# Optimization experiments

Hardware: AMD Instinct MI355X
Metric: run time of the kernel (lower is better)

The kernel has to match this reference:

```python
import jax, jax.numpy as jnp
import numpy as np
from jax import lax

NB_DIGITS = 2
BASE = 10
NUMS = BASE ** NB_DIGITS            # 100 possible values per number
SUMS = 2 * (NUMS - 1) + 1           # 199 possible sums (circuit roots)
B = 4096                            # logical batch size
N_IMAGES = B * 2 * NB_DIGITS        # 16384 digit images


def setup_inputs() -> dict:
    key = jax.random.key(0)
    ks = jax.random.split(key, 11)
    s = 0.1
    return {
        "images": jax.random.normal(ks[0], (N_IMAGES, 1, 28, 28), jnp.float32),
        "conv1_w": jax.random.normal(ks[1], (6, 1, 5, 5), jnp.float32) * s,
        "conv1_b": jax.random.normal(ks[2], (6,), jnp.float32) * s,
        "conv2_w": jax.random.normal(ks[3], (16, 6, 5, 5), jnp.float32) * s,
        "conv2_b": jax.random.normal(ks[4], (16,), jnp.float32) * s,
        "fc1_w": jax.random.normal(ks[5], (120, 256), jnp.float32) * s,
        "fc1_b": jax.random.normal(ks[6], (120,), jnp.float32) * s,
        "fc2_w": jax.random.normal(ks[7], (84, 120), jnp.float32) * s,
        "fc2_b": jax.random.normal(ks[8], (84,), jnp.float32) * s,
        "fc3_w": jax.random.normal(ks[9], (10, 84), jnp.float32) * s,
        "fc3_b": jax.random.normal(ks[10], (10,), jnp.float32) * s,
    }


def _conv(x, w, b):
    y = lax.conv_general_dilated(x, w, (1, 1), 'VALID',
                                 dimension_numbers=('NCHW', 'OIHW', 'NCHW'))
    return y + b[None, :, None, None]


def _maxpool2(x):
    return lax.reduce_window(x, -jnp.inf, lax.max, (1, 1, 2, 2), (1, 1, 2, 2), 'VALID')


def _lenet(x, c1w, c1b, c2w, c2b, f1w, f1b, f2w, f2b, f3w, f3b):
    x = jax.nn.relu(_maxpool2(_conv(x, c1w, c1b)))   # [N,6,12,12]
    x = jax.nn.relu(_maxpool2(_conv(x, c2w, c2b)))   # [N,16,4,4]
    x = x.reshape(-1, 16 * 4 * 4)
    x = jax.nn.relu(x @ f1w.T + f1b)
    x = jax.nn.relu(x @ f2w.T + f2b)
    x = x @ f3w.T + f3b
    return jax.nn.log_softmax(x, axis=-1)            # [N,10]


def _circuit(lp):
    # lp: [B, 2*NB_DIGITS, 10] per-digit log-probs.
    # Vars layout from get_circuit: positions 0..NB_DIGITS-1 = n1 digits (MSB first),
    # positions NB_DIGITS..2*NB_DIGITS-1 = n2 digits. Neg-literal weights are 0 in
    # log space (the `zeros` arg), so each model's weight = sum of digit log-probs;
    # OR over models = logsumexp grouped by n1+n2.
    d = jnp.arange(NUMS)
    hi, lo = d // BASE, d % BASE
    lp1 = lp[:, 0, hi] + lp[:, 1, lo]                # [B, NUMS] log P(n1=k)
    lp2 = lp[:, 2, hi] + lp[:, 3, lo]                # [B, NUMS] log P(n2=k)
    M = (lp1[:, :, None] + lp2[:, None, :]).reshape(lp.shape[0], -1)  # [B, NUMS^2]
    seg = (jnp.arange(NUMS)[:, None] + jnp.arange(NUMS)[None, :]).reshape(-1)
    Mf = M.T                                          # [NUMS^2, B]
    m = jax.ops.segment_max(Mf, seg, num_segments=SUMS)              # [SUMS, B]
    ssum = jax.ops.segment_sum(jnp.exp(Mf - m[seg]), seg, num_segments=SUMS)
    return (jnp.log(ssum) + m).T                      # [B, SUMS] log P(sum=s)


def reference(images, conv1_w, conv1_b, conv2_w, conv2_b,
              fc1_w, fc1_b, fc2_w, fc2_b, fc3_w, fc3_b):
    logp = _lenet(images, conv1_w, conv1_b, conv2_w, conv2_b,
                  fc1_w, fc1_b, fc2_w, fc2_b, fc3_w, fc3_b)   # [N_IMAGES,10]
    lp = logp.reshape(B, 2 * NB_DIGITS, BASE)
    return _circuit(lp)
```

## Files before the change

### kernel.cpp

```cpp
#include <hip/hip_runtime.h>
#include <hip/hip_bf16.h>
#include <math.h>

#define SUMS 199
#define NBLK 1024

typedef __attribute__((ext_vector_type(8))) short short8;
typedef __attribute__((ext_vector_type(4))) float float4v;

union Frag8 { short8 v; unsigned u[4]; uint4 q; };

static __device__ inline unsigned pk_bf16(float a, float b) {
    __hip_bfloat162 h = __float22bfloat162_rn(make_float2(a, b));
    union { __hip_bfloat162 h; unsigned u; } c; c.h = h; return c.u;
}

__global__ __launch_bounds__(256) void convert_weights(
    const float* __restrict__ f1w, const float* __restrict__ f2w,
    const float* __restrict__ f3w, const float* __restrict__ c1w,
    const float* __restrict__ c2w, uint4* __restrict__ ws)
{
    const int g = blockIdx.x * 256 + threadIdx.x;
    if (g >= 6400) return;
    float v[8];
    if (g < 5824) {
        const float* W; int O, K, ld, nt, s, l;
        if (g < 4096)      { W = f1w; O = 120; K = 256; ld = 256; nt = g >> 9; s = (g >> 6) & 7; l = g & 63; }
        else if (g < 5632) { const int f = g - 4096; W = f2w; O = 84; K = 120; ld = 120; nt = f >> 8; s = (f >> 6) & 3; l = f & 63; }
        else               { const int f = g - 5632; W = f3w; O = 10; K = 84;  ld = 84;  nt = 0; s = f >> 6; l = f & 63; }
        const int o = nt * 16 + (l & 15);
        #pragma unroll
        for (int j = 0; j < 8; ++j) {
            const int k = 32 * s + 8 * (l >> 4) + j;
            v[j] = (o < O && k < K) ? W[o * ld + k] : 0.f;
        }
    } else if (g < 6336) {
        const int f = g - 5824, s = f >> 6, l = f & 63;
        const int c = l & 15, h = l >> 4;
        #pragma unroll
        for (int jp = 0; jp < 4; ++jp) {
            const int D = 16 * s + 4 * h + jp;
            const int ky = D / 24, rem = D % 24, kx = rem >> 2, icp = rem & 3;
            const bool ok = (ky < 5 && kx < 5);
            v[2 * jp]     = (ok && 2 * icp < 6)     ? c2w[c * 150 + (2 * icp) * 25 + ky * 5 + kx]     : 0.f;
            v[2 * jp + 1] = (ok && 2 * icp + 1 < 6) ? c2w[c * 150 + (2 * icp + 1) * 25 + ky * 5 + kx] : 0.f;
        }
    } else {
        const int l = (g - 6336) & 63;
        const int c = l & 15, h = l >> 4;
        const int oc = c >> 1, xs = c & 1;
        #pragma unroll
        for (int j = 0; j < 8; ++j) {
            const int p = h * 4 + (j >> 1);
            float w = 0.f;
            if (p < 15 && c < 12) {
                const int ky = p / 3, kx = 2 * (p % 3) + (j & 1) - xs;
                if (kx >= 0 && kx < 5) w = c1w[oc * 25 + ky * 5 + kx];
            }
            v[j] = w;
        }
    }
    uint4 r;
    r.x = pk_bf16(v[0], v[1]); r.y = pk_bf16(v[2], v[3]);
    r.z = pk_bf16(v[4], v[5]); r.w = pk_bf16(v[6], v[7]);
    ws[g] = r;
}

__global__ __launch_bounds__(256) void lenet_circuit_kernel(
    const float* __restrict__ images,
    const float* __restrict__ c1b, const float* __restrict__ c2b,
    const float* __restrict__ f1b, const float* __restrict__ f2b,
    const float* __restrict__ f3b, const uint4* __restrict__ wsb,
    float* __restrict__ out)
{
    __shared__ __align__(16) unsigned char s_mem[39712];
    unsigned*       imgu = (unsigned*)s_mem;
    unsigned short* p1s  = (unsigned short*)(s_mem + 12576);
    const uint4*    p1u4 = (const uint4*)(s_mem + 12576);
    unsigned*       A1d  = (unsigned*)(s_mem + 31264);
    const uint4*    A1q  = (const uint4*)(s_mem + 31264);
    float*          pgf  = (float*)(s_mem + 7680);
    float*          Hf   = (float*)(s_mem + 8448);
    float*          Lf   = (float*)(s_mem + 8768);

    const int t = threadIdx.x, bid = blockIdx.x;
    const int lane = t & 63, wav = t >> 6;
    const int c = lane & 15, h = lane >> 4;
    const uint4 z4 = {0u, 0u, 0u, 0u};

    {
        uint4* pz = (uint4*)(s_mem + 12576);
        for (int i = t; i < 1168; i += 256) pz[i] = z4;
    }
    Frag8 a1; a1.q = wsb[6336 + lane];
    Frag8 w2[8];
    #pragma unroll
    for (int s = 0; s < 8; ++s) w2[s].q = wsb[5824 + s * 64 + lane];
    int koff[8];
    #pragma unroll
    for (int s = 0; s < 8; ++s) {
        const int D0 = 16 * s + 4 * h;
        koff[s] = (D0 / 24) * 12 + ((D0 % 24) >> 2);
    }
    int pd[4];
    #pragma unroll
    for (int q = 0; q < 4; ++q) {
        const int p = 4 * h + q;
        pd[q] = (p < 15) ? (p / 3) * 14 + (p % 3) : 0;
    }
    float bias0 = 0.f, bias1 = 0.f;
    if (h < 3) { bias0 = c1b[2 * h]; bias1 = c1b[2 * h + 1]; }
    const float b2v = c2b[c];

    for (int pass = 0; pass < 2; ++pass) {
        {
            const float4* g = (const float4*)(images + (size_t)bid * 12544 + pass * 6272);
            for (int i = t; i < 1568; i += 256) {
                const float4 v = g[i];
                const int im = i / 196, j = i % 196;
                imgu[im * 393 + 2 * j]     = pk_bf16(v.x, v.y);
                imgu[im * 393 + 2 * j + 1] = pk_bf16(v.z, v.w);
            }
        }
        __syncthreads();

        {
            const int n = c, img = n >> 1;
            const int imb = img * 393 + (n & 1) * 14;
            for (int qy = wav * 3; qy < wav * 3 + 3; ++qy) {
                #pragma unroll
                for (int qx = 0; qx < 12; ++qx) {
                    const int base = imb + qy * 28 + qx;
                    Frag8 bf;
                    #pragma unroll
                    for (int q = 0; q < 4; ++q) bf.u[q] = imgu[base + pd[q]];
                    float4v acc = {0.f, 0.f, 0.f, 0.f};
                    acc = __builtin_amdgcn_mfma_f32_16x16x32_bf16(a1.v, bf.v, acc, 0, 0, 0);
                    float v0 = fmaxf(acc[0], acc[1]);
                    float v1 = fmaxf(acc[2], acc[3]);
                    v0 = fmaxf(v0, __shfl_xor(v0, 1));
                    v1 = fmaxf(v1, __shfl_xor(v1, 1));
                    if ((n & 1) == 0 && h < 3) {
                        const unsigned pkv = pk_bf16(fmaxf(v0 + bias0, 0.f),
                                                     fmaxf(v1 + bias1, 0.f));
                        *(unsigned*)&p1s[img * 1152 + qy * 96 + qx * 8 + 2 * h] = pkv;
                    }
                }
            }
        }
        __syncthreads();

        {
            const int pxl = (c & 1) + 2 * ((c >> 2) & 1);
            const int pyl = ((c >> 1) & 1) + 2 * ((c >> 3) & 1);
            #pragma unroll
            for (int ii = 0; ii < 2; ++ii) {
                const int i0 = 2 * wav + ii;
                #pragma unroll
                for (int mt = 0; mt < 4; ++mt) {
                    const int px = pxl + 4 * (mt & 1), py = pyl + 4 * (mt >> 1);
                    const int base = i0 * 144 + py * 12 + px;
                    float4v acc = {0.f, 0.f, 0.f, 0.f};
                    #pragma unroll
                    for (int s = 0; s < 8; ++s) {
                        Frag8 af; af.q = p1u4[base + koff[s]];
                        acc = __builtin_amdgcn_mfma_f32_16x16x32_bf16(af.v, w2[s].v, acc, 0, 0, 0);
                    }
                    const float p = fmaxf(fmaxf(acc[0], acc[1]), fmaxf(acc[2], acc[3]));
                    float v = fmaxf(p + b2v, 0.f);
                    const float vp = __shfl_xor(v, 16);
                    if ((h & 1) == 0) {
                        const int qy = (h >> 1) + 2 * (mt >> 1);
                        A1d[(pass * 8 + i0) * 132 + c * 8 + qy * 2 + (mt & 1)] = pk_bf16(v, vp);
                    }
                }
            }
        }
    }
    __syncthreads();

    {
        unsigned* A2d = (unsigned*)s_mem;
        if (t < 64) A2d[(t >> 2) * 68 + 60 + (t & 3)] = 0u;
        float4v acc0 = {0.f, 0.f, 0.f, 0.f}, acc1 = acc0;
        const int nt0 = 2 * wav;
        #pragma unroll
        for (int s = 0; s < 8; ++s) {
            Frag8 af; af.q = A1q[c * 33 + 4 * s + h];
            Frag8 b0; b0.q = wsb[(nt0 * 8 + s) * 64 + lane];
            Frag8 b1; b1.q = wsb[((nt0 + 1) * 8 + s) * 64 + lane];
            acc0 = __builtin_amdgcn_mfma_f32_16x16x32_bf16(af.v, b0.v, acc0, 0, 0, 0);
            acc1 = __builtin_amdgcn_mfma_f32_16x16x32_bf16(af.v, b1.v, acc1, 0, 0, 0);
        }
        #pragma unroll
        for (int ntl = 0; ntl < 2; ++ntl) {
            const int o = 32 * wav + 16 * ntl + c;
            const float bias = (o < 120) ? f1b[o] : 0.f;
            #pragma unroll
            for (int r = 0; r < 4; ++r) {
                float v = fmaxf((ntl ? acc1[r] : acc0[r]) + bias, 0.f);
                const float vp = __shfl_xor(v, 1);
                if ((c & 1) == 0 && o < 120)
                    A2d[(4 * h + r) * 68 + (o >> 1)] = pk_bf16(v, vp);
            }
        }
    }
    __syncthreads();

    {
        unsigned* A3d = (unsigned*)(s_mem + 4352);
        if (t < 96) A3d[(t / 6) * 52 + 42 + (t % 6)] = 0u;
        if (wav < 3) {
            const uint4* A2q = (const uint4*)s_mem;
            float4v acc0 = {0.f, 0.f, 0.f, 0.f}, acc1 = acc0;
            const int nt0 = 2 * wav;
            #pragma unroll
            for (int s = 0; s < 4; ++s) {
                Frag8 af; af.q = A2q[c * 17 + 4 * s + h];
                Frag8 b0; b0.q = wsb[4096 + (nt0 * 4 + s) * 64 + lane];
                Frag8 b1; b1.q = wsb[4096 + ((nt0 + 1) * 4 + s) * 64 + lane];
                acc0 = __builtin_amdgcn_mfma_f32_16x16x32_bf16(af.v, b0.v, acc0, 0, 0, 0);
                acc1 = __builtin_amdgcn_mfma_f32_16x16x32_bf16(af.v, b1.v, acc1, 0, 0, 0);
            }
            #pragma unroll
            for (int ntl = 0; ntl < 2; ++ntl) {
                const int o = 32 * wav + 16 * ntl + c;
                const float bias = (o < 84) ? f2b[o] : 0.f;
                #pragma unroll
                for (int r = 0; r < 4; ++r) {
                    float v = fmaxf((ntl ? acc1[r] : acc0[r]) + bias, 0.f);
                    const float vp = __shfl_xor(v, 1);
                    if ((c & 1) == 0 && o < 84)
                        A3d[(4 * h + r) * 52 + (o >> 1)] = pk_bf16(v, vp);
                }
            }
        }
    }
    __syncthreads();

    if (wav == 0) {
        const uint4* A3q = (const uint4*)(s_mem + 4352);
        float4v acc = {0.f, 0.f, 0.f, 0.f};
        #pragma unroll
        for (int s = 0; s < 3; ++s) {
            Frag8 af; af.q = A3q[c * 13 + 4 * s + h];
            Frag8 b; b.q = wsb[5632 + s * 64 + lane];
            acc = __builtin_amdgcn_mfma_f32_16x16x32_bf16(af.v, b.v, acc, 0, 0, 0);
        }
        const float bias = (c < 10) ? f3b[c] : 0.f;
        float x[4], m[4], e[4], sm[4];
        #pragma unroll
        for (int r = 0; r < 4; ++r) {
            x[r] = (c < 10) ? (acc[r] + bias) : -INFINITY;
            m[r] = x[r];
        }
        #pragma unroll
        for (int d = 1; d <= 8; d <<= 1)
            #pragma unroll
            for (int r = 0; r < 4; ++r) m[r] = fmaxf(m[r], __shfl_xor(m[r], d));
        #pragma unroll
        for (int r = 0; r < 4; ++r) { e[r] = (c < 10) ? expf(x[r] - m[r]) : 0.f; sm[r] = e[r]; }
        #pragma unroll
        for (int d = 1; d <= 8; d <<= 1)
            #pragma unroll
            for (int r = 0; r < 4; ++r) sm[r] += __shfl_xor(sm[r], d);
        if (c < 10) {
            #pragma unroll
            for (int r = 0; r < 4; ++r)
                pgf[(4 * h + r) * 12 + c] = e[r] / sm[r];
        }
    }
    __syncthreads();

    if (t < 152) {
        const int be = t / 38, j = t % 38;
        const int isH = (j < 19), b = isH ? j : j - 19;
        const float* pg = pgf + 4 * be * 12;
        const float* PA = pg + (isH ? 0 : 12);
        const float* PB = pg + (isH ? 24 : 36);
        const int ilo = (b > 9) ? b - 9 : 0;
        const int ihi = (b < 9) ? b : 9;
        float s = 0.f;
        for (int i = ilo; i <= ihi; ++i) s += PA[i] * PB[b - i];
        (isH ? Hf : Lf)[be * 20 + b] = s;
    }
    __syncthreads();

    for (int idx = t; idx < 4 * SUMS; idx += 256) {
        const int be = idx / SUMS, s = idx % SUMS;
        const float* H = Hf + be * 20;
        const float* L = Lf + be * 20;
        const int bmin = (s > 18) ? (s - 9) / 10 : 0;
        int bmax = s / 10; if (bmax > 18) bmax = 18;
        float sum = 0.f;
        for (int b = bmin; b <= bmax; ++b) sum += H[b] * L[s - 10 * b];
        out[((size_t)bid * 4 + be) * SUMS + s] = logf(sum);
    }
}

extern "C" void kernel_launch(void* const* d_in, const int* in_sizes, int n_in,
                              void* d_out, int out_size, void* d_ws, size_t ws_size,
                              hipStream_t stream) {
    const float* images = (const float*)d_in[0];
    const float* c1w = (const float*)d_in[1];
    const float* c1b = (const float*)d_in[2];
    const float* c2w = (const float*)d_in[3];
    const float* c2b = (const float*)d_in[4];
    const float* f1w = (const float*)d_in[5];
    const float* f1b = (const float*)d_in[6];
    const float* f2w = (const float*)d_in[7];
    const float* f2b = (const float*)d_in[8];
    const float* f3w = (const float*)d_in[9];
    const float* f3b = (const float*)d_in[10];
    float* out = (float*)d_out;

    convert_weights<<<25, 256, 0, stream>>>(f1w, f2w, f3w, c1w, c2w, (uint4*)d_ws);
    lenet_circuit_kernel<<<NBLK, 256, 0, stream>>>(
        images, c1b, c2b, f1b, f2b, f3b, (const uint4*)d_ws, out);
}
```

Measured before the change: 138.8 us.

## Prefetch second image pass into registers and pack conv2 K dimension tighter

Loads the second pass's images into registers at kernel start so the global load latency overlaps with the first pass's conv1/conv2 work, removing one sync-bound load phase. It repacks conv2 weights so the K dimension is ordered as (spatial position, input channel pair), cutting conv2 from 8 to 7 MFMA steps per tile. The per-image pool1 stride changes from 144 to 145 uint4 to reduce LDS bank conflicts. It also raises launch bounds to 4 blocks per CU, which adds register pressure alongside the 7 float4 prefetch registers and could cause spills.

```diff
diff --git a/kernel.cpp b/kernel.cpp
--- a/kernel.cpp
+++ b/kernel.cpp
@@ -37,13 +37,13 @@
     } else if (g < 6336) {
         const int f = g - 5824, s = f >> 6, l = f & 63;
         const int c = l & 15, h = l >> 4;
+        const int pos = 4 * s + h;
+        const int ky = pos / 5, kx = pos % 5;
+        const bool ok = (pos < 25);
         #pragma unroll
         for (int jp = 0; jp < 4; ++jp) {
-            const int D = 16 * s + 4 * h + jp;
-            const int ky = D / 24, rem = D % 24, kx = rem >> 2, icp = rem & 3;
-            const bool ok = (ky < 5 && kx < 5);
-            v[2 * jp]     = (ok && 2 * icp < 6)     ? c2w[c * 150 + (2 * icp) * 25 + ky * 5 + kx]     : 0.f;
-            v[2 * jp + 1] = (ok && 2 * icp + 1 < 6) ? c2w[c * 150 + (2 * icp + 1) * 25 + ky * 5 + kx] : 0.f;
+            v[2 * jp]     = (ok && 2 * jp < 6)     ? c2w[c * 150 + (2 * jp) * 25 + ky * 5 + kx]     : 0.f;
+            v[2 * jp + 1] = (ok && 2 * jp + 1 < 6) ? c2w[c * 150 + (2 * jp + 1) * 25 + ky * 5 + kx] : 0.f;
         }
     } else {
         const int l = (g - 6336) & 63;
@@ -66,7 +66,7 @@
     ws[g] = r;
 }
 
-__global__ __launch_bounds__(256) void lenet_circuit_kernel(
+__global__ __launch_bounds__(256, 4) void lenet_circuit_kernel(
     const float* __restrict__ images,
     const float* __restrict__ c1b, const float* __restrict__ c2b,
     const float* __restrict__ f1b, const float* __restrict__ f2b,
@@ -93,14 +93,14 @@
         for (int i = t; i < 1168; i += 256) pz[i] = z4;
     }
     Frag8 a1; a1.q = wsb[6336 + lane];
-    Frag8 w2[8];
+    Frag8 w2[7];
     #pragma unroll
-    for (int s = 0; s < 8; ++s) w2[s].q = wsb[5824 + s * 64 + lane];
-    int koff[8];
+    for (int s = 0; s < 7; ++s) w2[s].q = wsb[5824 + s * 64 + lane];
+    int koff[7];
     #pragma unroll
-    for (int s = 0; s < 8; ++s) {
-        const int D0 = 16 * s + 4 * h;
-        koff[s] = (D0 / 24) * 12 + ((D0 % 24) >> 2);
+    for (int s = 0; s < 7; ++s) {
+        const int pos = 4 * s + h;
+        koff[s] = (pos < 25) ? (pos / 5) * 12 + (pos % 5) : 0;
     }
     int pd[4];
     #pragma unroll
@@ -112,71 +112,97 @@
     if (h < 3) { bias0 = c1b[2 * h]; bias1 = c1b[2 * h + 1]; }
     const float b2v = c2b[c];
 
-    for (int pass = 0; pass < 2; ++pass) {
-        {
-            const float4* g = (const float4*)(images + (size_t)bid * 12544 + pass * 6272);
-            for (int i = t; i < 1568; i += 256) {
-                const float4 v = g[i];
-                const int im = i / 196, j = i % 196;
-                imgu[im * 393 + 2 * j]     = pk_bf16(v.x, v.y);
-                imgu[im * 393 + 2 * j + 1] = pk_bf16(v.z, v.w);
-            }
-        }
-        __syncthreads();
-
-        {
-            const int n = c, img = n >> 1;
-            const int imb = img * 393 + (n & 1) * 14;
-            for (int qy = wav * 3; qy < wav * 3 + 3; ++qy) {
+    float4 pf[7];
+    {
+        const float4* g1 = (const float4*)(images + (size_t)bid * 12544 + 6272);
+        #pragma unroll
+        for (int k = 0; k < 6; ++k) pf[k] = g1[t + 256 * k];
+        if (t < 32) pf[6] = g1[1536 + t];
+    }
+
+    auto do_conv1 = [&]() {
+        const int n = c, img = n >> 1;
+        const int imb = img * 393 + (n & 1) * 14;
+        for (int qy = wav * 3; qy < wav * 3 + 3; ++qy) {
+            #pragma unroll
+            for (int qx = 0; qx < 12; ++qx) {
+                const int base = imb + qy * 28 + qx;
+                Frag8 bf;
                 #pragma unroll
-                for (int qx = 0; qx < 12; ++qx) {
-                    const int base = imb + qy * 28 + qx;
-                    Frag8 bf;
-                    #pragma unroll
-                    for (int q = 0; q < 4; ++q) bf.u[q] = imgu[base + pd[q]];
-                    float4v acc = {0.f, 0.f, 0.f, 0.f};
-                    acc = __builtin_amdgcn_mfma_f32_16x16x32_bf16(a1.v, bf.v, acc, 0, 0, 0);
-                    float v0 = fmaxf(acc[0], acc[1]);
-                    float v1 = fmaxf(acc[2], acc[3]);
-                    v0 = fmaxf(v0, __shfl_xor(v0, 1));
-                    v1 = fmaxf(v1, __shfl_xor(v1, 1));
-                    if ((n & 1) == 0 && h < 3) {
-                        const unsigned pkv = pk_bf16(fmaxf(v0 + bias0, 0.f),
-                                                     fmaxf(v1 + bias1, 0.f));
-                        *(unsigned*)&p1s[img * 1152 + qy * 96 + qx * 8 + 2 * h] = pkv;
-                    }
+                for (int q = 0; q < 4; ++q) bf.u[q] = imgu[base + pd[q]];
+                float4v acc = {0.f, 0.f, 0.f, 0.f};
+                acc = __builtin_amdgcn_mfma_f32_16x16x32_bf16(a1.v, bf.v, acc, 0, 0, 0);
+                float v0 = fmaxf(acc[0], acc[1]);
+                float v1 = fmaxf(acc[2], acc[3]);
+                v0 = fmaxf(v0, __shfl_xor(v0, 1));
+                v1 = fmaxf(v1, __shfl_xor(v1, 1));
+                if ((n & 1) == 0 && h < 3) {
+                    const unsigned pkv = pk_bf16(fmaxf(v0 + bias0, 0.f),
+                                                 fmaxf(v1 + bias1, 0.f));
+                    *(unsigned*)&p1s[img * 1160 + qy * 96 + qx * 8 + 2 * h] = pkv;
                 }
             }
         }
-        __syncthreads();
-
-        {
-            const int pxl = (c & 1) + 2 * ((c >> 2) & 1);
-            const int pyl = ((c >> 1) & 1) + 2 * ((c >> 3) & 1);
-            #pragma unroll
-            for (int ii = 0; ii < 2; ++ii) {
-                const int i0 = 2 * wav + ii;
+    };
+    auto do_conv2 = [&](int pass) {
+        const int pxl = (c & 1) + 2 * ((c >> 2) & 1);
+        const int pyl = ((c >> 1) & 1) + 2 * ((c >> 3) & 1);
+        #pragma unroll
+        for (int ii = 0; ii < 2; ++ii) {
+            const int i0 = 2 * wav + ii;
+            #pragma unroll
+            for (int mt = 0; mt < 4; ++mt) {
+                const int px = pxl + 4 * (mt & 1), py = pyl + 4 * (mt >> 1);
+                const int base = i0 * 145 + py * 12 + px;
+                float4v acc = {0.f, 0.f, 0.f, 0.f};
                 #pragma unroll
-                for (int mt = 0; mt < 4; ++mt) {
-                    const int px = pxl + 4 * (mt & 1), py = pyl + 4 * (mt >> 1);
-                    const int base = i0 * 144 + py * 12 + px;
-                    float4v acc = {0.f, 0.f, 0.f, 0.f};
-                    #pragma unroll
-                    for (int s = 0; s < 8; ++s) {
-                        Frag8 af; af.q = p1u4[base + koff[s]];
-                        acc = __builtin_amdgcn_mfma_f32_16x16x32_bf16(af.v, w2[s].v, acc, 0, 0, 0);
-                    }
-                    const float p = fmaxf(fmaxf(acc[0], acc[1]), fmaxf(acc[2], acc[3]));
-                    float v = fmaxf(p + b2v, 0.f);
-                    const float vp = __shfl_xor(v, 16);
-                    if ((h & 1) == 0) {
-                        const int qy = (h >> 1) + 2 * (mt >> 1);
-                        A1d[(pass * 8 + i0) * 132 + c * 8 + qy * 2 + (mt & 1)] = pk_bf16(v, vp);
-                    }
+                for (int s = 0; s < 7; ++s) {
+                    Frag8 af; af.q = p1u4[base + koff[s]];
+                    acc = __builtin_amdgcn_mfma_f32_16x16x32_bf16(af.v, w2[s].v, acc, 0, 0, 0);
                 }
-            }
-        }
-    }
+                const float p = fmaxf(fmaxf(acc[0], acc[1]), fmaxf(acc[2], acc[3]));
+                float v = fmaxf(p + b2v, 0.f);
+                const float vp = __shfl_xor(v, 16);
+                if ((h & 1) == 0) {
+                    const int qy = (h >> 1) + 2 * (mt >> 1);
+                    A1d[(pass * 8 + i0) * 132 + c * 8 + qy * 2 + (mt & 1)] = pk_bf16(v, vp);
+                }
+            }
+        }
+    };
+
+    {
+        const float4* g = (const float4*)(images + (size_t)bid * 12544);
+        for (int i = t; i < 1568; i += 256) {
+            const float4 v = g[i];
+            const int im = i / 196, j = i % 196;
+            imgu[im * 393 + 2 * j]     = pk_bf16(v.x, v.y);
+            imgu[im * 393 + 2 * j + 1] = pk_bf16(v.z, v.w);
+        }
+    }
+    __syncthreads();
+    do_conv1();
+    __syncthreads();
+    do_conv2(0);
+    {
+        #pragma unroll
+        for (int k = 0; k < 6; ++k) {
+            const int i = t + 256 * k;
+            const int im = i / 196, j = i % 196;
+            imgu[im * 393 + 2 * j]     = pk_bf16(pf[k].x, pf[k].y);
+            imgu[im * 393 + 2 * j + 1] = pk_bf16(pf[k].z, pf[k].w);
+        }
+        if (t < 32) {
+            const int i = 1536 + t;
+            const int im = i / 196, j = i % 196;
+            imgu[im * 393 + 2 * j]     = pk_bf16(pf[6].x, pf[6].y);
+            imgu[im * 393 + 2 * j + 1] = pk_bf16(pf[6].z, pf[6].w);
+        }
+    }
+    __syncthreads();
+    do_conv1();
+    __syncthreads();
+    do_conv2(1);
     __syncthreads();
 
     {
```

After: 135.4 us. 2.4% less time.
